# Optimization experiments

Measured on AMD Instinct MI355X. Metric: run time of the kernel, lower is better.

The kernel has to match this reference:

```python
import jax, jax.numpy as jnp
import numpy as np

NUM_HEADS = 64
NUM_KV_HEADS = 8
HEAD_DIM = 128
Q_MULT = NUM_HEADS // NUM_KV_HEADS  # 8
CACHE_LEN = 8192
SLIDING_WINDOW = 4096
BATCH = 16
SM_SCALE = 1.0 / float(np.sqrt(HEAD_DIM))


def setup_inputs() -> dict:
    key = jax.random.key(0)
    k1, k2, k3, k4, k5 = jax.random.split(key, 5)
    return {
        "Q": jax.random.normal(k1, (BATCH, 1, NUM_HEADS * HEAD_DIM), dtype=jnp.float32),
        "K": jax.random.normal(k2, (BATCH, 1, NUM_KV_HEADS * HEAD_DIM), dtype=jnp.float32),
        "V": jax.random.normal(k3, (BATCH, 1, NUM_KV_HEADS * HEAD_DIM), dtype=jnp.float32),
        "K_cache": jax.random.normal(k4, (BATCH, CACHE_LEN, NUM_KV_HEADS * HEAD_DIM), dtype=jnp.float32),
        "V_cache": jax.random.normal(k5, (BATCH, CACHE_LEN, NUM_KV_HEADS * HEAD_DIM), dtype=jnp.float32),
        "sinks": jnp.zeros((NUM_HEADS,), dtype=jnp.float32),
    }


def reference(Q, K, V, K_cache, V_cache, sinks):
    B = Q.shape[0]
    total_len = CACHE_LEN + 1
    # reshape to (B, kv_heads, q_mult, d) / (B, len, kv_heads, d)
    q = Q.reshape(B, NUM_KV_HEADS, Q_MULT, HEAD_DIM)
    k_new = K.reshape(B, 1, NUM_KV_HEADS, HEAD_DIM)
    v_new = V.reshape(B, 1, NUM_KV_HEADS, HEAD_DIM)
    k_full = jnp.concatenate([K_cache.reshape(B, CACHE_LEN, NUM_KV_HEADS, HEAD_DIM), k_new], axis=1)
    v_full = jnp.concatenate([V_cache.reshape(B, CACHE_LEN, NUM_KV_HEADS, HEAD_DIM), v_new], axis=1)

    # scores: (B, kv_heads, q_mult, total_len) -- GQA: each kv head serves q_mult query heads
    qk = jnp.einsum("bhmd,bkhd->bhmk", q, k_full) * SM_SCALE

    # sliding-window mask (static shapes: total_len > window here)
    if SLIDING_WINDOW > 0 and total_len > SLIDING_WINDOW:
        pos = jnp.arange(total_len)
        qk = jnp.where(pos[None, None, None, :] < total_len - SLIDING_WINDOW, -jnp.inf, qk)

    # append sink logit per query head, softmax, then drop sink column
    s = sinks.reshape(1, NUM_KV_HEADS, Q_MULT, 1)
    logits = jnp.concatenate([qk, jnp.broadcast_to(s, (B, NUM_KV_HEADS, Q_MULT, 1))], axis=-1)
    w = jax.nn.softmax(logits, axis=-1)[..., :-1]

    attn = jnp.einsum("bhmk,bkhd->bhmd", w, v_full)
    return attn.reshape(B, 1, NUM_HEADS * HEAD_DIM)
```

## Files before the change

### kernel.cpp

```cpp
#include <hip/hip_runtime.h>
#include <math.h>

#define BATCH 16
#define KVH 8
#define QM 8
#define NH 64
#define HD 128
#define CACHE 8192
#define WIN 4096
#define TOTAL (CACHE + 1)
#define PSTART (TOTAL - WIN)
#define TILE 64
#define KSTRIDE (KVH * HD)
#define LDSTR 132
#define REC_FLOATS (QM * (HD + 2))

template <int NC>
__global__ __launch_bounds__(256, 4)
void attn_partial(const float* __restrict__ Q,
                  const float* __restrict__ Knew,
                  const float* __restrict__ Vnew,
                  const float* __restrict__ Kc,
                  const float* __restrict__ Vc,
                  float* __restrict__ ws) {
    constexpr int CL = WIN / NC;
    const int c   = blockIdx.x;
    const int kvh = blockIdx.y;
    const int b   = blockIdx.z;
    const int t   = threadIdx.x;

    __shared__ float q_s[QM][HD];
    __shared__ float kv_s[TILE][LDSTR];
    __shared__ float w_s[QM][TILE];

    {
        const float* qp = Q + ((size_t)b * NH + kvh * QM) * HD;
        for (int i = t; i < QM * HD; i += 256)
            q_s[i / HD][i % HD] = qp[i] * 0.08838834764831845f;
    }
    __syncthreads();

    const int h  = t >> 5;
    const int lp = t & 31;

    float acc0 = 0.f, acc1 = 0.f, acc2 = 0.f, acc3 = 0.f;
    float m_run = -INFINITY;
    float l_run = 0.f;

    const size_t cache_base = (size_t)b * CACHE * KSTRIDE + (size_t)kvh * HD;
    const size_t new_base   = (size_t)b * KSTRIDE + (size_t)kvh * HD;
    const int p_base = PSTART + c * CL;

    for (int tb = 0; tb < CL; tb += TILE) {
        for (int i = t; i < TILE * (HD / 4); i += 256) {
            int r = i >> 5;
            int g = i & 31;
            int p = p_base + tb + r;
            const float* src = (p < CACHE) ? (Kc + cache_base + (size_t)p * KSTRIDE)
                                           : (Knew + new_base);
            float4 v = *reinterpret_cast<const float4*>(src + g * 4);
            *reinterpret_cast<float4*>(&kv_s[r][g * 4]) = v;
        }
        __syncthreads();

        float s0 = 0.f, s1 = 0.f;
        {
            const float* qrow = q_s[h];
            const float* k0 = kv_s[lp];
            const float* k1 = kv_s[lp + 32];
            #pragma unroll
            for (int d = 0; d < HD; d += 4) {
                float4 qv  = *reinterpret_cast<const float4*>(qrow + d);
                float4 kv0 = *reinterpret_cast<const float4*>(k0 + d);
                float4 kv1 = *reinterpret_cast<const float4*>(k1 + d);
                s0 += qv.x * kv0.x + qv.y * kv0.y + qv.z * kv0.z + qv.w * kv0.w;
                s1 += qv.x * kv1.x + qv.y * kv1.y + qv.z * kv1.z + qv.w * kv1.w;
            }
        }

        float mt = fmaxf(s0, s1);
        #pragma unroll
        for (int off = 16; off; off >>= 1) mt = fmaxf(mt, __shfl_xor(mt, off));
        float m_new = fmaxf(m_run, mt);
        float e0 = __expf(s0 - m_new);
        float e1 = __expf(s1 - m_new);
        float rs = __expf(m_run - m_new);
        float lsum = e0 + e1;
        #pragma unroll
        for (int off = 16; off; off >>= 1) lsum += __shfl_xor(lsum, off);
        l_run = l_run * rs + lsum;
        m_run = m_new;
        acc0 *= rs; acc1 *= rs; acc2 *= rs; acc3 *= rs;
        w_s[h][lp]      = e0;
        w_s[h][lp + 32] = e1;
        __syncthreads();

        for (int i = t; i < TILE * (HD / 4); i += 256) {
            int r = i >> 5;
            int g = i & 31;
            int p = p_base + tb + r;
            const float* src = (p < CACHE) ? (Vc + cache_base + (size_t)p * KSTRIDE)
                                           : (Vnew + new_base);
            float4 v = *reinterpret_cast<const float4*>(src + g * 4);
            *reinterpret_cast<float4*>(&kv_s[r][g * 4]) = v;
        }
        __syncthreads();

        #pragma unroll 4
        for (int p = 0; p < TILE; ++p) {
            float wv = w_s[h][p];
            acc0 += wv * kv_s[p][lp];
            acc1 += wv * kv_s[p][lp + 32];
            acc2 += wv * kv_s[p][lp + 64];
            acc3 += wv * kv_s[p][lp + 96];
        }
        __syncthreads();
    }

    float* rec = ws + (size_t)((b * KVH + kvh) * NC + c) * REC_FLOATS;
    if (lp == 0) { rec[h] = m_run; rec[QM + h] = l_run; }
    float* accp = rec + 2 * QM + h * HD;
    accp[lp]      = acc0;
    accp[lp + 32] = acc1;
    accp[lp + 64] = acc2;
    accp[lp + 96] = acc3;
}

template <int NC>
__global__ __launch_bounds__(256)
void attn_combine(const float* __restrict__ ws,
                  const float* __restrict__ sinks,
                  float* __restrict__ out) {
    const int kvh = blockIdx.x;
    const int b   = blockIdx.y;
    const int t   = threadIdx.x;
    const int h   = t >> 5;
    const int lp  = t & 31;

    const float* base = ws + (size_t)((b * KVH + kvh) * NC) * REC_FLOATS;
    const float sk = sinks[kvh * QM + h];

    float m[NC], l[NC];
    float M = sk;
    #pragma unroll
    for (int c = 0; c < NC; ++c) {
        m[c] = base[(size_t)c * REC_FLOATS + h];
        l[c] = base[(size_t)c * REC_FLOATS + QM + h];
        M = fmaxf(M, m[c]);
    }
    float denom = __expf(sk - M);
    float wgt[NC];
    #pragma unroll
    for (int c = 0; c < NC; ++c) {
        wgt[c] = __expf(m[c] - M);
        denom += wgt[c] * l[c];
    }
    float inv = 1.f / denom;

    float o0 = 0.f, o1 = 0.f, o2 = 0.f, o3 = 0.f;
    #pragma unroll
    for (int c = 0; c < NC; ++c) {
        const float* accp = base + (size_t)c * REC_FLOATS + 2 * QM + h * HD;
        o0 += wgt[c] * accp[lp];
        o1 += wgt[c] * accp[lp + 32];
        o2 += wgt[c] * accp[lp + 64];
        o3 += wgt[c] * accp[lp + 96];
    }
    float* op = out + (size_t)b * NH * HD + (size_t)(kvh * QM + h) * HD;
    op[lp]      = o0 * inv;
    op[lp + 32] = o1 * inv;
    op[lp + 64] = o2 * inv;
    op[lp + 96] = o3 * inv;
}

template <int NC>
static void launch_nc(const float* Q, const float* K, const float* V,
                      const float* Kc, const float* Vc, const float* sinks,
                      float* out, float* ws, hipStream_t stream) {
    dim3 g1(NC, KVH, BATCH);
    attn_partial<NC><<<g1, 256, 0, stream>>>(Q, K, V, Kc, Vc, ws);
    dim3 g2(KVH, BATCH);
    attn_combine<NC><<<g2, 256, 0, stream>>>(ws, sinks, out);
}

extern "C" void kernel_launch(void* const* d_in, const int* in_sizes, int n_in,
                              void* d_out, int out_size, void* d_ws, size_t ws_size,
                              hipStream_t stream) {
    const float* Q     = (const float*)d_in[0];
    const float* K     = (const float*)d_in[1];
    const float* V     = (const float*)d_in[2];
    const float* Kc    = (const float*)d_in[3];
    const float* Vc    = (const float*)d_in[4];
    const float* sinks = (const float*)d_in[5];
    float* out = (float*)d_out;
    float* ws  = (float*)d_ws;

    auto need = [](int nc) {
        return (size_t)BATCH * KVH * nc * REC_FLOATS * sizeof(float);
    };
    if (ws_size >= need(8))      launch_nc<8>(Q, K, V, Kc, Vc, sinks, out, ws, stream);
    else if (ws_size >= need(4)) launch_nc<4>(Q, K, V, Kc, Vc, sinks, out, ws, stream);
    else if (ws_size >= need(2)) launch_nc<2>(Q, K, V, Kc, Vc, sinks, out, ws, stream);
    else                         launch_nc<1>(Q, K, V, Kc, Vc, sinks, out, ws, stream);
}
```

Before: 121.2 us.

## Rewrite split-K decode attention to register-resident per-wave streaming without LDS tiles

Replaces the LDS-tiled, barrier-heavy partial kernel with one where each wave keeps Q and its accumulators in registers and streams K/V rows directly from global memory with a one-step prefetch. Each half-wave handles its own positions, scores are reduced with a butterfly shuffle transpose, and the online softmax is rescaled lazily, only when the max grows by more than a threshold. Waves are merged through a small LDS combine, and the split count rises to 16 when the workspace allows it. The aim is to remove the per-tile __syncthreads and LDS traffic and to expose more memory parallelism, at the cost of higher register pressure and extra shuffles.

```diff
diff --git a/kernel.cpp b/kernel.cpp
--- a/kernel.cpp
+++ b/kernel.cpp
@@ -10,12 +10,97 @@
 #define WIN 4096
 #define TOTAL (CACHE + 1)
 #define PSTART (TOTAL - WIN)
-#define TILE 64
 #define KSTRIDE (KVH * HD)
-#define LDSTR 132
 #define REC_FLOATS (QM * (HD + 2))
-
-template <int NC>
+#define SM_SCALE 0.08838834764831845f
+
+
+template <bool EDGE>
+__device__ __forceinline__ void run_span(
+    const float4 q4[8], float4 acc[8], float& mrun, float& lrun,
+    const float* kc, const float* vc, const float* kn, const float* vn,
+    int pb, int nstep, int ln) {
+
+    auto loadK = [&](int p) -> float4 {
+        const float* src = (!EDGE || p < CACHE) ? (kc + (size_t)p * KSTRIDE) : kn;
+        return *reinterpret_cast<const float4*>(src);
+    };
+    auto loadV = [&](int p) -> float4 {
+        const float* src = (!EDGE || p < CACHE) ? (vc + (size_t)p * KSTRIDE) : vn;
+        return *reinterpret_cast<const float4*>(src);
+    };
+
+    const int dp = ln & 31;
+    float4 k4 = loadK(pb);
+    float4 v4 = loadV(pb);
+
+    for (int j = 0; j < nstep; ++j) {
+        float4 kcur = k4, vcur = v4;
+        if (j + 1 < nstep) {
+            int pn = pb + 2 * (j + 1);
+            k4 = loadK(pn);
+            v4 = loadV(pn);
+        }
+
+        float part[8];
+        #pragma unroll
+        for (int h = 0; h < 8; ++h)
+            part[h] = q4[h].x * kcur.x + q4[h].y * kcur.y +
+                      q4[h].z * kcur.z + q4[h].w * kcur.w;
+
+        float f4[4];
+        {
+            const bool s1 = dp & 1;
+            #pragma unroll
+            for (int i = 0; i < 4; ++i) {
+                float send = s1 ? part[2*i]   : part[2*i+1];
+                float keep = s1 ? part[2*i+1] : part[2*i];
+                f4[i] = keep + __shfl_xor(send, 1);
+            }
+        }
+        float f2[2];
+        {
+            const bool s2 = dp & 2;
+            #pragma unroll
+            for (int i = 0; i < 2; ++i) {
+                float send = s2 ? f4[2*i]   : f4[2*i+1];
+                float keep = s2 ? f4[2*i+1] : f4[2*i];
+                f2[i] = keep + __shfl_xor(send, 2);
+            }
+        }
+        float s;
+        {
+            const bool s4 = dp & 4;
+            float send = s4 ? f2[0] : f2[1];
+            float keep = s4 ? f2[1] : f2[0];
+            s = keep + __shfl_xor(send, 4);
+        }
+        s += __shfl_xor(s, 8);
+        s += __shfl_xor(s, 16);
+
+        if (__any(s > mrun + 8.0f)) {
+            float mn = fmaxf(mrun, s);
+            float rs = __expf(mrun - mn);
+            mrun = mn;
+            lrun *= rs;
+            #pragma unroll
+            for (int h = 0; h < 8; ++h) {
+                float rh = __shfl(rs, (ln & 0x20) | h);
+                acc[h].x *= rh; acc[h].y *= rh; acc[h].z *= rh; acc[h].w *= rh;
+            }
+        }
+        float e = __expf(s - mrun);
+        lrun += e;
+        #pragma unroll
+        for (int h = 0; h < 8; ++h) {
+            float wh = __shfl(e, (ln & 0x20) | h);
+            acc[h].x += wh * vcur.x; acc[h].y += wh * vcur.y;
+            acc[h].z += wh * vcur.z; acc[h].w += wh * vcur.w;
+        }
+    }
+}
+
+template <int NSPLIT>
 __global__ __launch_bounds__(256, 4)
 void attn_partial(const float* __restrict__ Q,
                   const float* __restrict__ Knew,
@@ -23,107 +108,101 @@
                   const float* __restrict__ Kc,
                   const float* __restrict__ Vc,
                   float* __restrict__ ws) {
-    constexpr int CL = WIN / NC;
+    constexpr int SPAN  = WIN / NSPLIT;
+    constexpr int WSPAN = SPAN / 4;
+    constexpr int NSTEP = WSPAN / 2;
+
     const int c   = blockIdx.x;
     const int kvh = blockIdx.y;
     const int b   = blockIdx.z;
     const int t   = threadIdx.x;
-
-    __shared__ float q_s[QM][HD];
-    __shared__ float kv_s[TILE][LDSTR];
-    __shared__ float w_s[QM][TILE];
-
+    const int wid = t >> 6;
+    const int ln  = t & 63;
+    const int dp  = ln & 31;
+    const int d0  = dp * 4;
+
+    float4 q4[8];
     {
-        const float* qp = Q + ((size_t)b * NH + kvh * QM) * HD;
-        for (int i = t; i < QM * HD; i += 256)
-            q_s[i / HD][i % HD] = qp[i] * 0.08838834764831845f;
+        const float* qp = Q + ((size_t)b * NH + (size_t)kvh * QM) * HD + d0;
+        #pragma unroll
+        for (int h = 0; h < 8; ++h) {
+            float4 v = *reinterpret_cast<const float4*>(qp + h * HD);
+            q4[h] = make_float4(v.x * SM_SCALE, v.y * SM_SCALE,
+                                v.z * SM_SCALE, v.w * SM_SCALE);
+        }
+    }
+
+    const int hi = ln >> 5;
+    const int pb = PSTART + c * SPAN + wid * WSPAN + hi;
+
+    const float* kc = Kc + (size_t)b * CACHE * KSTRIDE + (size_t)kvh * HD + d0;
+    const float* vc = Vc + (size_t)b * CACHE * KSTRIDE + (size_t)kvh * HD + d0;
+    const float* kn = Knew + (size_t)b * KSTRIDE + (size_t)kvh * HD + d0;
+    const float* vn = Vnew + (size_t)b * KSTRIDE + (size_t)kvh * HD + d0;
+
+    float4 acc[8];
+    #pragma unroll
+    for (int h = 0; h < 8; ++h) acc[h] = make_float4(0.f, 0.f, 0.f, 0.f);
+    float mrun = -INFINITY;
+    float lrun = 0.f;
+
+    if (pb + 2 * NSTEP - 2 >= CACHE)
+        run_span<true >(q4, acc, mrun, lrun, kc, vc, kn, vn, pb, NSTEP, ln);
+    else
+        run_span<false>(q4, acc, mrun, lrun, kc, vc, kn, vn, pb, NSTEP, ln);
+
+    {
+        float mo = __shfl_xor(mrun, 32);
+        float lo = __shfl_xor(lrun, 32);
+        float M  = fmaxf(mrun, mo);
+        float f  = __expf(mrun - M);
+        float fo = __expf(mo - M);
+        lrun = lrun * f + lo * fo;
+        mrun = M;
+        #pragma unroll
+        for (int h = 0; h < 8; ++h) {
+            float fh  = __shfl(f,  (ln & 0x20) | h);
+            float foh = __shfl(fo, (ln & 0x20) | h);
+            float ax = __shfl_xor(acc[h].x, 32);
+            float ay = __shfl_xor(acc[h].y, 32);
+            float az = __shfl_xor(acc[h].z, 32);
+            float aw = __shfl_xor(acc[h].w, 32);
+            acc[h].x = acc[h].x * fh + ax * foh;
+            acc[h].y = acc[h].y * fh + ay * foh;
+            acc[h].z = acc[h].z * fh + az * foh;
+            acc[h].w = acc[h].w * fh + aw * foh;
+        }
+    }
+
+    __shared__ float  sm_m[4][8];
+    __shared__ float  sm_l[4][8];
+    __shared__ float4 sm_a[4][8][32];
+
+    if (ln < 32) {
+        if (dp < 8) { sm_m[wid][dp] = mrun; sm_l[wid][dp] = lrun; }
+        #pragma unroll
+        for (int h = 0; h < 8; ++h) sm_a[wid][h][dp] = acc[h];
     }
     __syncthreads();
 
     const int h  = t >> 5;
-    const int lp = t & 31;
-
-    float acc0 = 0.f, acc1 = 0.f, acc2 = 0.f, acc3 = 0.f;
-    float m_run = -INFINITY;
-    float l_run = 0.f;
-
-    const size_t cache_base = (size_t)b * CACHE * KSTRIDE + (size_t)kvh * HD;
-    const size_t new_base   = (size_t)b * KSTRIDE + (size_t)kvh * HD;
-    const int p_base = PSTART + c * CL;
-
-    for (int tb = 0; tb < CL; tb += TILE) {
-        for (int i = t; i < TILE * (HD / 4); i += 256) {
-            int r = i >> 5;
-            int g = i & 31;
-            int p = p_base + tb + r;
-            const float* src = (p < CACHE) ? (Kc + cache_base + (size_t)p * KSTRIDE)
-                                           : (Knew + new_base);
-            float4 v = *reinterpret_cast<const float4*>(src + g * 4);
-            *reinterpret_cast<float4*>(&kv_s[r][g * 4]) = v;
-        }
-        __syncthreads();
-
-        float s0 = 0.f, s1 = 0.f;
-        {
-            const float* qrow = q_s[h];
-            const float* k0 = kv_s[lp];
-            const float* k1 = kv_s[lp + 32];
-            #pragma unroll
-            for (int d = 0; d < HD; d += 4) {
-                float4 qv  = *reinterpret_cast<const float4*>(qrow + d);
-                float4 kv0 = *reinterpret_cast<const float4*>(k0 + d);
-                float4 kv1 = *reinterpret_cast<const float4*>(k1 + d);
-                s0 += qv.x * kv0.x + qv.y * kv0.y + qv.z * kv0.z + qv.w * kv0.w;
-                s1 += qv.x * kv1.x + qv.y * kv1.y + qv.z * kv1.z + qv.w * kv1.w;
-            }
-        }
-
-        float mt = fmaxf(s0, s1);
-        #pragma unroll
-        for (int off = 16; off; off >>= 1) mt = fmaxf(mt, __shfl_xor(mt, off));
-        float m_new = fmaxf(m_run, mt);
-        float e0 = __expf(s0 - m_new);
-        float e1 = __expf(s1 - m_new);
-        float rs = __expf(m_run - m_new);
-        float lsum = e0 + e1;
-        #pragma unroll
-        for (int off = 16; off; off >>= 1) lsum += __shfl_xor(lsum, off);
-        l_run = l_run * rs + lsum;
-        m_run = m_new;
-        acc0 *= rs; acc1 *= rs; acc2 *= rs; acc3 *= rs;
-        w_s[h][lp]      = e0;
-        w_s[h][lp + 32] = e1;
-        __syncthreads();
-
-        for (int i = t; i < TILE * (HD / 4); i += 256) {
-            int r = i >> 5;
-            int g = i & 31;
-            int p = p_base + tb + r;
-            const float* src = (p < CACHE) ? (Vc + cache_base + (size_t)p * KSTRIDE)
-                                           : (Vnew + new_base);
-            float4 v = *reinterpret_cast<const float4*>(src + g * 4);
-            *reinterpret_cast<float4*>(&kv_s[r][g * 4]) = v;
-        }
-        __syncthreads();
-
-        #pragma unroll 4
-        for (int p = 0; p < TILE; ++p) {
-            float wv = w_s[h][p];
-            acc0 += wv * kv_s[p][lp];
-            acc1 += wv * kv_s[p][lp + 32];
-            acc2 += wv * kv_s[p][lp + 64];
-            acc3 += wv * kv_s[p][lp + 96];
-        }
-        __syncthreads();
-    }
-
-    float* rec = ws + (size_t)((b * KVH + kvh) * NC + c) * REC_FLOATS;
-    if (lp == 0) { rec[h] = m_run; rec[QM + h] = l_run; }
-    float* accp = rec + 2 * QM + h * HD;
-    accp[lp]      = acc0;
-    accp[lp + 32] = acc1;
-    accp[lp + 64] = acc2;
-    accp[lp + 96] = acc3;
+    const int dd = t & 31;
+    float mv[4];
+    float M = -INFINITY;
+    #pragma unroll
+    for (int i = 0; i < 4; ++i) { mv[i] = sm_m[i][h]; M = fmaxf(M, mv[i]); }
+    float lt = 0.f;
+    float4 o = make_float4(0.f, 0.f, 0.f, 0.f);
+    #pragma unroll
+    for (int i = 0; i < 4; ++i) {
+        float f = __expf(mv[i] - M);
+        lt += sm_l[i][h] * f;
+        float4 a = sm_a[i][h][dd];
+        o.x += a.x * f; o.y += a.y * f; o.z += a.z * f; o.w += a.w * f;
+    }
+    float* rec = ws + (size_t)((b * KVH + kvh) * NSPLIT + c) * REC_FLOATS;
+    if (dd == 0) { rec[h] = M; rec[QM + h] = lt; }
+    *reinterpret_cast<float4*>(rec + 2 * QM + h * HD + 4 * dd) = o;
 }
 
 template <int NC>
@@ -157,30 +236,27 @@
     }
     float inv = 1.f / denom;
 
-    float o0 = 0.f, o1 = 0.f, o2 = 0.f, o3 = 0.f;
+    float4 o = make_float4(0.f, 0.f, 0.f, 0.f);
     #pragma unroll
     for (int c = 0; c < NC; ++c) {
         const float* accp = base + (size_t)c * REC_FLOATS + 2 * QM + h * HD;
-        o0 += wgt[c] * accp[lp];
-        o1 += wgt[c] * accp[lp + 32];
-        o2 += wgt[c] * accp[lp + 64];
-        o3 += wgt[c] * accp[lp + 96];
+        float4 a = *reinterpret_cast<const float4*>(accp + 4 * lp);
+        o.x += wgt[c] * a.x; o.y += wgt[c] * a.y;
+        o.z += wgt[c] * a.z; o.w += wgt[c] * a.w;
     }
     float* op = out + (size_t)b * NH * HD + (size_t)(kvh * QM + h) * HD;
-    op[lp]      = o0 * inv;
-    op[lp + 32] = o1 * inv;
-    op[lp + 64] = o2 * inv;
-    op[lp + 96] = o3 * inv;
-}
-
-template <int NC>
+    float4 r = make_float4(o.x * inv, o.y * inv, o.z * inv, o.w * inv);
+    *reinterpret_cast<float4*>(op + 4 * lp) = r;
+}
+
+template <int NSPLIT>
 static void launch_nc(const float* Q, const float* K, const float* V,
                       const float* Kc, const float* Vc, const float* sinks,
                       float* out, float* ws, hipStream_t stream) {
-    dim3 g1(NC, KVH, BATCH);
-    attn_partial<NC><<<g1, 256, 0, stream>>>(Q, K, V, Kc, Vc, ws);
+    dim3 g1(NSPLIT, KVH, BATCH);
+    attn_partial<NSPLIT><<<g1, 256, 0, stream>>>(Q, K, V, Kc, Vc, ws);
     dim3 g2(KVH, BATCH);
-    attn_combine<NC><<<g2, 256, 0, stream>>>(ws, sinks, out);
+    attn_combine<NSPLIT><<<g2, 256, 0, stream>>>(ws, sinks, out);
 }
 
 extern "C" void kernel_launch(void* const* d_in, const int* in_sizes, int n_in,
@@ -198,8 +274,8 @@
     auto need = [](int nc) {
         return (size_t)BATCH * KVH * nc * REC_FLOATS * sizeof(float);
     };
-    if (ws_size >= need(8))      launch_nc<8>(Q, K, V, Kc, Vc, sinks, out, ws, stream);
+    if (ws_size >= need(16))     launch_nc<16>(Q, K, V, Kc, Vc, sinks, out, ws, stream);
+    else if (ws_size >= need(8)) launch_nc<8>(Q, K, V, Kc, Vc, sinks, out, ws, stream);
     else if (ws_size >= need(4)) launch_nc<4>(Q, K, V, Kc, Vc, sinks, out, ws, stream);
-    else if (ws_size >= need(2)) launch_nc<2>(Q, K, V, Kc, Vc, sinks, out, ws, stream);
-    else                         launch_nc<1>(Q, K, V, Kc, Vc, sinks, out, ws, stream);
-}
+    else                         launch_nc<2>(Q, K, V, Kc, Vc, sinks, out, ws, stream);
+}
```

After: 155.2 us. 28.1% more time.
